# Kernel optimization log

Measured on AMD Instinct MI355X. Metric: run time of the kernel, lower is better.

The kernel has to match this reference:

```python
import jax, jax.numpy as jnp
import numpy as np

NEG_SLOPE = 0.2  # PyG GATv2Conv default

N_NODES = 10000
N_EDGES = 320000
DIM_IN = 128
DIM_H = 32
HEADS = 8
DIM_OUT = 32
HID = DIM_H * HEADS  # 256


def _gatv2(x, src, dst, Wl, Wr, att, bias, heads, ch, n):
    # x: [N, Fin]; src/dst: [E] (self-loops already included)
    xl = (x @ Wl).reshape(n, heads, ch)  # source-side transform
    xr = (x @ Wr).reshape(n, heads, ch)  # target-side transform
    e = jax.nn.leaky_relu(xl[src] + xr[dst], NEG_SLOPE)       # [E, H, C]
    score = jnp.einsum('ehc,hc->eh', e, att)                  # [E, H]
    m = jax.ops.segment_max(score, dst, num_segments=n)        # [N, H]
    ex = jnp.exp(score - m[dst])
    denom = jax.ops.segment_sum(ex, dst, num_segments=n)
    alpha = ex / (denom[dst] + 1e-16)                          # [E, H]
    out = jax.ops.segment_sum(alpha[:, :, None] * xl[src], dst, num_segments=n)
    return out.reshape(n, heads * ch) + bias


def setup_inputs() -> dict:
    key = jax.random.key(0)
    ks = jax.random.split(key, 16)
    x = jax.random.normal(ks[0], (N_NODES, DIM_IN), dtype=jnp.float32)
    edge_index = jax.random.randint(ks[1], (2, N_EDGES), 0, N_NODES, dtype=jnp.int64)

    def glorot(k, shape, fan_in):
        return jax.random.normal(k, shape, dtype=jnp.float32) * (1.0 / np.sqrt(fan_in))

    return {
        'x': x,
        'W1l': glorot(ks[2], (DIM_IN, HID), DIM_IN),
        'W1r': glorot(ks[3], (DIM_IN, HID), DIM_IN),
        'a1': glorot(ks[4], (HEADS, DIM_H), DIM_H),
        'b1': jnp.zeros((HID,), dtype=jnp.float32),
        'W2l': glorot(ks[5], (HID, HID), HID),
        'W2r': glorot(ks[6], (HID, HID), HID),
        'a2': glorot(ks[7], (HEADS, DIM_H), DIM_H),
        'b2': jnp.zeros((HID,), dtype=jnp.float32),
        'W3l': glorot(ks[8], (HID, DIM_OUT), HID),
        'W3r': glorot(ks[9], (HID, DIM_OUT), HID),
        'a3': glorot(ks[10], (1, DIM_OUT), DIM_OUT),
        'b3': jnp.zeros((DIM_OUT,), dtype=jnp.float32),
        'edge_index': edge_index,
    }


def reference(x, W1l, W1r, a1, b1, W2l, W2r, a2, b2, W3l, W3r, a3, b3, edge_index):
    n = x.shape[0]
    loops = jnp.arange(n, dtype=edge_index.dtype)
    src = jnp.concatenate([edge_index[0], loops])
    dst = jnp.concatenate([edge_index[1], loops])

    # eval mode: dropout(p=0.6) is identity
    h = _gatv2(x, src, dst, W1l, W1r, a1, b1, HEADS, DIM_H, n)
    h = jax.nn.relu(h)
    h_res = h
    h = _gatv2(h, src, dst, W2l, W2r, a2, b2, HEADS, DIM_H, n)
    h = h + h_res
    h = _gatv2(h, src, dst, W3l, W3r, a3, b3, 1, DIM_OUT, n)
    return h
```

## Files before the change

kernel.cpp:

```cpp
#include <hip/hip_runtime.h>

#define N_NODES 10000
#define N_EDGES 320000
#define E_TOT   (N_EDGES + N_NODES)
#define HID 256
#define NEG_SLOPE 0.2f
#define SLOTS 192

typedef __attribute__((ext_vector_type(8))) short short8;
typedef __attribute__((ext_vector_type(4))) float float4v;

__device__ int   g_cnt[N_NODES];
__device__ int   g_csr[(size_t)N_NODES * SLOTS];
__device__ __align__(16) float g_xl[(size_t)N_NODES * HID];
__device__ __align__(16) float g_xr[(size_t)N_NODES * HID];
__device__ __align__(16) float g_h1[(size_t)N_NODES * HID];
__device__ __align__(16) unsigned short g_xlb[(size_t)N_NODES * HID];
__device__ __align__(16) unsigned short g_abf[(size_t)N_NODES * 512];
__device__ __align__(16) unsigned short g_bp1a[16 * 8  * 64 * 8];
__device__ __align__(16) unsigned short g_bp2a[16 * 8  * 64 * 8];
__device__ __align__(16) unsigned short g_bp1b[16 * 16 * 64 * 8];
__device__ __align__(16) unsigned short g_bp2b[16 * 16 * 64 * 8];
__device__ __align__(16) unsigned short g_bp1c[2  * 16 * 64 * 8];
__device__ __align__(16) unsigned short g_bp2c[2  * 16 * 64 * 8];

#define LOG2E 1.44269504088896340736f

__device__ __forceinline__ unsigned short f2bf(float f) {
    unsigned int u = __float_as_uint(f);
    unsigned int r = (u + 0x7fffu + ((u >> 16) & 1u)) >> 16;
    return (unsigned short)r;
}
__device__ __forceinline__ float bf2f(unsigned short h) {
    return __uint_as_float(((unsigned int)h) << 16);
}
__device__ __forceinline__ unsigned int splitpack(float f) {
    unsigned short hi = f2bf(f);
    unsigned short lo = f2bf(f - bf2f(hi));
    return ((unsigned int)lo << 16) | hi;
}

__device__ __forceinline__ void packB(const float* __restrict__ B,
                                      unsigned short* __restrict__ Bp,
                                      int t, int nkc, int N) {
    int lane = t & 63;
    int kc   = (t >> 6) % nkc;
    int nt   = (t >> 6) / nkc;
    int n = nt * 16 + (lane & 15);
    int kbase = kc * 32 + (lane >> 4) * 8;
    #pragma unroll
    for (int j = 0; j < 8; ++j) {
        int kp = kbase + j;
        int k  = kp >> 1;
        float f = B[(size_t)k * N + n];
        unsigned short hi = f2bf(f);
        Bp[(size_t)t * 8 + j] = (kp & 1) ? f2bf(f - bf2f(hi)) : hi;
    }
}

__global__ __launch_bounds__(256) void k_prep(const float* __restrict__ W1l,
                                              const float* __restrict__ W1r,
                                              int* __restrict__ cnt) {
    const int S0 = 16 * 8 * 64;
    int t = blockIdx.x * blockDim.x + threadIdx.x;
    if (t < S0) {
        packB(W1l, g_bp1a, t, 8, 256);
        packB(W1r, g_bp2a, t, 8, 256);
    } else {
        int u = t - S0;
        if (u < N_NODES) cnt[u] = 0;
    }
}

#define FILL_BLOCKS  ((E_TOT + 255) / 256)
#define GEMM1_BLOCKS ((N_NODES + 31) / 32)
#define PACK2_BLOCKS ((16 * 16 * 64 + 2 * 16 * 64 + 255) / 256)
__global__ __launch_bounds__(256) void k_fill_gemm1(
    const int* __restrict__ ei,
    int* __restrict__ cnt, int* __restrict__ csr,
    const float4* __restrict__ A4,
    const short8* __restrict__ Bp1, const short8* __restrict__ Bp2,
    unsigned short* __restrict__ C1b,
    float* __restrict__ C2,
    const float* __restrict__ W2l, const float* __restrict__ W2r,
    const float* __restrict__ W3l, const float* __restrict__ W3r)
{
    if (blockIdx.x < FILL_BLOCKS) {
        int e = blockIdx.x * 256 + threadIdx.x;
        if (e < E_TOT) {
            int src, dst;
            if (e < N_EDGES) { src = ei[e]; dst = ei[N_EDGES + e]; }
            else             { src = dst = e - N_EDGES; }
            int pos = atomicAdd(&cnt[dst], 1);
            if (pos < SLOTS) csr[dst * SLOTS + pos] = src;
        }
        return;
    }
    if (blockIdx.x >= FILL_BLOCKS + GEMM1_BLOCKS) {
        const int S1 = 16 * 16 * 64;
        const int S2 = 2 * 16 * 64;
        int t = (blockIdx.x - FILL_BLOCKS - GEMM1_BLOCKS) * 256 + threadIdx.x;
        if (t < S1) {
            packB(W2l, g_bp1b, t, 16, 256);
            packB(W2r, g_bp2b, t, 16, 256);
        } else {
            int u = t - S1;
            if (u < S2) {
                packB(W3l, g_bp1c, u, 16, 32);
                packB(W3r, g_bp2c, u, 16, 32);
            }
        }
        return;
    }
    const int nkc = 8;
    int mt   = blockIdx.x - FILL_BLOCKS;
    int lane = threadIdx.x & 63;
    int wid  = threadIdx.x >> 6;
    int quad = lane >> 4;
    int col  = lane & 15;
    int r0 = mt * 32 + col;       if (r0 >= N_NODES) r0 = N_NODES - 1;
    int r1 = mt * 32 + 16 + col;  if (r1 >= N_NODES) r1 = N_NODES - 1;
    const float4* a0 = A4 + (size_t)r0 * 32 + quad;
    const float4* a1 = A4 + (size_t)r1 * 32 + quad;
    float4v acc[2][4][2];
    #pragma unroll
    for (int s = 0; s < 2; ++s)
        #pragma unroll
        for (int t = 0; t < 4; ++t) { acc[s][t][0] = (float4v)(0.f); acc[s][t][1] = (float4v)(0.f); }
    for (int kc = 0; kc < nkc; ++kc) {
        float4 v0 = a0[kc * 4];
        float4 v1 = a1[kc * 4];
        union { short8 s; unsigned int u[4]; } c0, c1;
        c0.u[0] = splitpack(v0.x); c0.u[1] = splitpack(v0.y);
        c0.u[2] = splitpack(v0.z); c0.u[3] = splitpack(v0.w);
        c1.u[0] = splitpack(v1.x); c1.u[1] = splitpack(v1.y);
        c1.u[2] = splitpack(v1.z); c1.u[3] = splitpack(v1.w);
        short8 A0 = c0.s, A1 = c1.s;
        #pragma unroll
        for (int t = 0; t < 4; ++t) {
            int nt = wid * 4 + t;
            size_t bi = ((size_t)(nt * nkc + kc)) * 64 + lane;
            short8 b1 = Bp1[bi];
            short8 b2 = Bp2[bi];
            acc[0][t][0] = __builtin_amdgcn_mfma_f32_16x16x32_bf16(A0, b1, acc[0][t][0], 0, 0, 0);
            acc[0][t][1] = __builtin_amdgcn_mfma_f32_16x16x32_bf16(A0, b2, acc[0][t][1], 0, 0, 0);
            acc[1][t][0] = __builtin_amdgcn_mfma_f32_16x16x32_bf16(A1, b1, acc[1][t][0], 0, 0, 0);
            acc[1][t][1] = __builtin_amdgcn_mfma_f32_16x16x32_bf16(A1, b2, acc[1][t][1], 0, 0, 0);
        }
    }
    #pragma unroll
    for (int s = 0; s < 2; ++s) {
        #pragma unroll
        for (int t = 0; t < 4; ++t) {
            int gc = (wid * 4 + t) * 16 + col;
            #pragma unroll
            for (int r = 0; r < 4; ++r) {
                int row = mt * 32 + s * 16 + quad * 4 + r;
                if (row < N_NODES) {
                    C1b[(size_t)row * 256 + gc] = f2bf(acc[s][t][0][r]);
                    C2[(size_t)row * 256 + gc]  = acc[s][t][1][r];
                }
            }
        }
    }
}

__global__ __launch_bounds__(256) void k_mgemm2(const short8* __restrict__ Af,
                                                const short8* __restrict__ Bp1,
                                                const short8* __restrict__ Bp2,
                                                unsigned short* __restrict__ C1b,
                                                float* __restrict__ C2,
                                                int Kp, int nkc) {
    int mt   = blockIdx.x;
    int lane = threadIdx.x & 63;
    int wid  = threadIdx.x >> 6;
    int quad = lane >> 4;
    int col  = lane & 15;
    int ks   = Kp >> 3;
    int r0 = mt * 32 + col;       if (r0 >= N_NODES) r0 = N_NODES - 1;
    int r1 = mt * 32 + 16 + col;  if (r1 >= N_NODES) r1 = N_NODES - 1;
    const short8* a0 = Af + (size_t)r0 * ks + quad;
    const short8* a1 = Af + (size_t)r1 * ks + quad;
    float4v acc[2][4][2];
    #pragma unroll
    for (int s = 0; s < 2; ++s)
        #pragma unroll
        for (int t = 0; t < 4; ++t) { acc[s][t][0] = (float4v)(0.f); acc[s][t][1] = (float4v)(0.f); }
    for (int kc = 0; kc < nkc; ++kc) {
        short8 A0 = a0[kc * 4];
        short8 A1 = a1[kc * 4];
        #pragma unroll
        for (int t = 0; t < 4; ++t) {
            int nt = wid * 4 + t;
            size_t bi = ((size_t)(nt * nkc + kc)) * 64 + lane;
            short8 b1 = Bp1[bi];
            short8 b2 = Bp2[bi];
            acc[0][t][0] = __builtin_amdgcn_mfma_f32_16x16x32_bf16(A0, b1, acc[0][t][0], 0, 0, 0);
            acc[0][t][1] = __builtin_amdgcn_mfma_f32_16x16x32_bf16(A0, b2, acc[0][t][1], 0, 0, 0);
            acc[1][t][0] = __builtin_amdgcn_mfma_f32_16x16x32_bf16(A1, b1, acc[1][t][0], 0, 0, 0);
            acc[1][t][1] = __builtin_amdgcn_mfma_f32_16x16x32_bf16(A1, b2, acc[1][t][1], 0, 0, 0);
        }
    }
    #pragma unroll
    for (int s = 0; s < 2; ++s) {
        #pragma unroll
        for (int t = 0; t < 4; ++t) {
            int gc = (wid * 4 + t) * 16 + col;
            #pragma unroll
            for (int r = 0; r < 4; ++r) {
                int row = mt * 32 + s * 16 + quad * 4 + r;
                if (row < N_NODES) {
                    C1b[(size_t)row * 256 + gc] = f2bf(acc[s][t][0][r]);
                    C2[(size_t)row * 256 + gc]  = acc[s][t][1][r];
                }
            }
        }
    }
}

__global__ __launch_bounds__(256) void k_mgemm32(const short8* __restrict__ Af,
                                                 const short8* __restrict__ Bp1,
                                                 const short8* __restrict__ Bp2,
                                                 float* __restrict__ C1,
                                                 float* __restrict__ C2) {
    int mt   = blockIdx.x;
    int lane = threadIdx.x & 63;
    int wid  = threadIdx.x >> 6;
    int quad = lane >> 4;
    int col  = lane & 15;
    int nt   = wid & 1;
    const short8* Bp = (wid < 2) ? Bp1 : Bp2;
    float* C = (wid < 2) ? C1 : C2;

    const short8* abase = Af + (size_t)(mt * 16 + col) * 64 + quad;
    float4v acc = (float4v)(0.f);
    #pragma unroll 4
    for (int kc = 0; kc < 16; ++kc) {
        short8 a = abase[kc * 4];
        short8 b = Bp[((size_t)(nt * 16 + kc)) * 64 + lane];
        acc = __builtin_amdgcn_mfma_f32_16x16x32_bf16(a, b, acc, 0, 0, 0);
    }
    #pragma unroll
    for (int r = 0; r < 4; ++r)
        C[(size_t)(mt * 16 + quad * 4 + r) * 32 + nt * 16 + col] = acc[r];
}

__global__ __launch_bounds__(256) void k_agg8(const unsigned short* __restrict__ xlb,
                                              const float4* __restrict__ xr4,
                                              const float4* __restrict__ att4,
                                              const float4* __restrict__ bias4,
                                              const int* __restrict__ cnt,
                                              const int* __restrict__ csr_src,
                                              const float4* __restrict__ res4,
                                              float4* __restrict__ out4,
                                              uint4* __restrict__ abf_out,
                                              int mode) {
    int node = blockIdx.x * 4 + (threadIdx.x >> 6);
    if (node >= N_NODES) return;
    int lane = threadIdx.x & 63;
    float4 xrv = xr4[(size_t)node * 64 + lane];
    float4 av  = att4[lane];
    av.x *= LOG2E; av.y *= LOG2E; av.z *= LOG2E; av.w *= LOG2E;
    int c = cnt[node]; if (c > SLOTS) c = SLOTS;
    int base0 = node * SLOTS;

    float s = 0.f;
    float4 acc = make_float4(0.f, 0.f, 0.f, 0.f);

    for (int base = 0; base < c; base += 64) {
        int li = base + lane;
        int idxv = csr_src[base0 + (li < c ? li : c - 1)];
        int m = c - base; if (m > 64) m = 64;
        for (int j0 = 0; j0 < m; j0 += 4) {
            int srcs[4];
            ushort4 uv[4];
            #pragma unroll
            for (int j = 0; j < 4; ++j)
                srcs[j] = __shfl(idxv, j0 + j);
            #pragma unroll
            for (int j = 0; j < 4; ++j)
                uv[j] = *(const ushort4*)(xlb + (size_t)srcs[j] * 256 + 4 * lane);
            #pragma unroll
            for (int j = 0; j < 4; ++j) {
                if (j0 + j < m) {
                    float4 xv;
                    xv.x = bf2f(uv[j].x); xv.y = bf2f(uv[j].y);
                    xv.z = bf2f(uv[j].z); xv.w = bf2f(uv[j].w);
                    float tx = xv.x + xrv.x, ty = xv.y + xrv.y;
                    float tz = xv.z + xrv.z, tw = xv.w + xrv.w;
                    float w = fmaxf(tx, NEG_SLOPE * tx) * av.x
                            + fmaxf(ty, NEG_SLOPE * ty) * av.y
                            + fmaxf(tz, NEG_SLOPE * tz) * av.z
                            + fmaxf(tw, NEG_SLOPE * tw) * av.w;
                    w += __shfl_xor(w, 1);
                    w += __shfl_xor(w, 2);
                    w += __shfl_xor(w, 4);
                    float p = exp2f(w);
                    s += p;
                    acc.x += p * xv.x;
                    acc.y += p * xv.y;
                    acc.z += p * xv.z;
                    acc.w += p * xv.w;
                }
            }
        }
    }

    float inv = 1.f / (s + 1e-16f);
    float4 bv = bias4[lane];
    float4 o;
    o.x = acc.x * inv + bv.x; o.y = acc.y * inv + bv.y;
    o.z = acc.z * inv + bv.z; o.w = acc.w * inv + bv.w;
    if (mode == 0) {
        o.x = fmaxf(o.x, 0.f); o.y = fmaxf(o.y, 0.f);
        o.z = fmaxf(o.z, 0.f); o.w = fmaxf(o.w, 0.f);
    } else {
        float4 r = res4[(size_t)node * 64 + lane];
        o.x += r.x; o.y += r.y; o.z += r.z; o.w += r.w;
    }
    if (out4) out4[(size_t)node * 64 + lane] = o;
    if (abf_out) {
        uint4 u;
        u.x = splitpack(o.x); u.y = splitpack(o.y);
        u.z = splitpack(o.z); u.w = splitpack(o.w);
        abf_out[(size_t)node * 64 + lane] = u;
    }
}

__global__ __launch_bounds__(256) void k_agg1(const float4* __restrict__ xl4,
                                              const float4* __restrict__ xr4,
                                              const float4* __restrict__ att4,
                                              const float4* __restrict__ bias4,
                                              const int* __restrict__ cnt,
                                              const int* __restrict__ csr_src,
                                              float4* __restrict__ out4) {
    int node = blockIdx.x * 4 + (threadIdx.x >> 6);
    if (node >= N_NODES) return;
    int lane = threadIdx.x & 63;
    int q = lane & 7;
    int grp = lane >> 3;
    float4 xrv = xr4[(size_t)node * 8 + q];
    float4 av  = att4[q];
    av.x *= LOG2E; av.y *= LOG2E; av.z *= LOG2E; av.w *= LOG2E;
    int c = cnt[node]; if (c > SLOTS) c = SLOTS;
    int start = node * SLOTS, end = start + c;
    float s = 0.f;
    float4 acc = make_float4(0.f, 0.f, 0.f, 0.f);
    for (int i = start + grp; i < end; i += 8) {
        int src = csr_src[i];
        float4 xv = xl4[(size_t)src * 8 + q];
        float tx = xv.x + xrv.x, ty = xv.y + xrv.y;
        float tz = xv.z + xrv.z, tw = xv.w + xrv.w;
        float w = fmaxf(tx, NEG_SLOPE * tx) * av.x
                + fmaxf(ty, NEG_SLOPE * ty) * av.y
                + fmaxf(tz, NEG_SLOPE * tz) * av.z
                + fmaxf(tw, NEG_SLOPE * tw) * av.w;
        w += __shfl_xor(w, 1);
        w += __shfl_xor(w, 2);
        w += __shfl_xor(w, 4);
        float p = exp2f(w);
        s += p;
        acc.x += p * xv.x;
        acc.y += p * xv.y;
        acc.z += p * xv.z;
        acc.w += p * xv.w;
    }
    #pragma unroll
    for (int off = 8; off < 64; off <<= 1) {
        s     += __shfl_xor(s, off);
        acc.x += __shfl_xor(acc.x, off);
        acc.y += __shfl_xor(acc.y, off);
        acc.z += __shfl_xor(acc.z, off);
        acc.w += __shfl_xor(acc.w, off);
    }
    if (grp == 0) {
        float inv = 1.f / (s + 1e-16f);
        float4 bv = bias4[q];
        float4 o;
        o.x = acc.x * inv + bv.x; o.y = acc.y * inv + bv.y;
        o.z = acc.z * inv + bv.z; o.w = acc.w * inv + bv.w;
        out4[(size_t)node * 8 + q] = o;
    }
}


extern "C" void kernel_launch(void* const* d_in, const int* in_sizes, int n_in,
                              void* d_out, int out_size, void* d_ws, size_t ws_size,
                              hipStream_t stream) {
    const float* x   = (const float*)d_in[0];
    const float* W1l = (const float*)d_in[1];
    const float* W1r = (const float*)d_in[2];
    const float* a1  = (const float*)d_in[3];
    const float* b1  = (const float*)d_in[4];
    const float* W2l = (const float*)d_in[5];
    const float* W2r = (const float*)d_in[6];
    const float* a2  = (const float*)d_in[7];
    const float* b2  = (const float*)d_in[8];
    const float* W3l = (const float*)d_in[9];
    const float* W3r = (const float*)d_in[10];
    const float* a3  = (const float*)d_in[11];
    const float* b3  = (const float*)d_in[12];
    const int*   ei  = (const int*)d_in[13];
    float* out = (float*)d_out;

    int *cnt, *csr;
    float *xl, *xr, *h1;
    unsigned short *xlb, *abf, *bp1a, *bp2a, *bp1b, *bp2b, *bp1c, *bp2c;
    hipGetSymbolAddress((void**)&cnt,    HIP_SYMBOL(g_cnt));
    hipGetSymbolAddress((void**)&csr,    HIP_SYMBOL(g_csr));
    hipGetSymbolAddress((void**)&xl,     HIP_SYMBOL(g_xl));
    hipGetSymbolAddress((void**)&xr,     HIP_SYMBOL(g_xr));
    hipGetSymbolAddress((void**)&h1,     HIP_SYMBOL(g_h1));
    hipGetSymbolAddress((void**)&xlb,    HIP_SYMBOL(g_xlb));
    hipGetSymbolAddress((void**)&abf,    HIP_SYMBOL(g_abf));
    hipGetSymbolAddress((void**)&bp1a,   HIP_SYMBOL(g_bp1a));
    hipGetSymbolAddress((void**)&bp2a,   HIP_SYMBOL(g_bp2a));
    hipGetSymbolAddress((void**)&bp1b,   HIP_SYMBOL(g_bp1b));
    hipGetSymbolAddress((void**)&bp2b,   HIP_SYMBOL(g_bp2b));
    hipGetSymbolAddress((void**)&bp1c,   HIP_SYMBOL(g_bp1c));
    hipGetSymbolAddress((void**)&bp2c,   HIP_SYMBOL(g_bp2c));

    k_prep<<<(16 * 8 * 64 + N_NODES + 255) / 256, 256, 0, stream>>>(W1l, W1r, cnt);

    k_fill_gemm1<<<FILL_BLOCKS + GEMM1_BLOCKS + PACK2_BLOCKS, 256, 0, stream>>>(
        ei, cnt, csr, (const float4*)x,
        (const short8*)bp1a, (const short8*)bp2a, xlb, xr,
        W2l, W2r, W3l, W3r);

    k_agg8<<<(N_NODES + 3) / 4, 256, 0, stream>>>(xlb, (const float4*)xr,
                                        (const float4*)a1, (const float4*)b1,
                                        cnt, csr, nullptr, (float4*)h1,
                                        (uint4*)abf, 0);

    k_mgemm2<<<(N_NODES + 31) / 32, 256, 0, stream>>>((const short8*)abf,
                                                      (const short8*)bp1b, (const short8*)bp2b,
                                                      xlb, xr, 512, 16);

    k_agg8<<<(N_NODES + 3) / 4, 256, 0, stream>>>(xlb, (const float4*)xr,
                                        (const float4*)a2, (const float4*)b2,
                                        cnt, csr, (const float4*)h1, nullptr,
                                        (uint4*)abf, 1);

    k_mgemm32<<<N_NODES / 16, 256, 0, stream>>>((const short8*)abf,
                                                (const short8*)bp1c, (const short8*)bp2c,
                                                xl, xr);

    k_agg1<<<(N_NODES + 3) / 4, 256, 0, stream>>>((const float4*)xl, (const float4*)xr,
                                                  (const float4*)a3, (const float4*)b3,
                                                  cnt, csr, (float4*)out);
}
```

Measured before the change: 227.1 us.

## Fuse GAT aggregation with following layer GEMM via shared-memory tile

```diff
diff --git a/kernel.cpp b/kernel.cpp
--- a/kernel.cpp
+++ b/kernel.cpp
@@ -16,7 +16,7 @@
 __device__ __align__(16) float g_xr[(size_t)N_NODES * HID];
 __device__ __align__(16) float g_h1[(size_t)N_NODES * HID];
 __device__ __align__(16) unsigned short g_xlb[(size_t)N_NODES * HID];
-__device__ __align__(16) unsigned short g_abf[(size_t)N_NODES * 512];
+__device__ __align__(16) unsigned short g_xlb2[(size_t)N_NODES * HID];
 __device__ __align__(16) unsigned short g_bp1a[16 * 8  * 64 * 8];
 __device__ __align__(16) unsigned short g_bp2a[16 * 8  * 64 * 8];
 __device__ __align__(16) unsigned short g_bp1b[16 * 16 * 64 * 8];
@@ -165,165 +165,151 @@
     }
 }
 
-__global__ __launch_bounds__(256) void k_mgemm2(const short8* __restrict__ Af,
-                                                const short8* __restrict__ Bp1,
-                                                const short8* __restrict__ Bp2,
+__global__ __launch_bounds__(512) void k_aggemm(const unsigned short* __restrict__ xlb,
+                                                const float4* __restrict__ xr4,
+                                                const float4* __restrict__ att4,
+                                                const float4* __restrict__ bias4,
+                                                const int* __restrict__ cnt,
+                                                const int* __restrict__ csr_src,
+                                                const float4* __restrict__ res4,
+                                                float4* __restrict__ h1out,
+                                                const short8* __restrict__ BpA,
+                                                const short8* __restrict__ BpB,
                                                 unsigned short* __restrict__ C1b,
                                                 float* __restrict__ C2,
-                                                int Kp, int nkc) {
-    int mt   = blockIdx.x;
+                                                float* __restrict__ C1f,
+                                                int mode) {
+    __shared__ uint4 sp[16][64];
     int lane = threadIdx.x & 63;
     int wid  = threadIdx.x >> 6;
     int quad = lane >> 4;
     int col  = lane & 15;
-    int ks   = Kp >> 3;
-    int r0 = mt * 32 + col;       if (r0 >= N_NODES) r0 = N_NODES - 1;
-    int r1 = mt * 32 + 16 + col;  if (r1 >= N_NODES) r1 = N_NODES - 1;
-    const short8* a0 = Af + (size_t)r0 * ks + quad;
-    const short8* a1 = Af + (size_t)r1 * ks + quad;
-    float4v acc[2][4][2];
-    #pragma unroll
-    for (int s = 0; s < 2; ++s)
-        #pragma unroll
-        for (int t = 0; t < 4; ++t) { acc[s][t][0] = (float4v)(0.f); acc[s][t][1] = (float4v)(0.f); }
-    for (int kc = 0; kc < nkc; ++kc) {
-        short8 A0 = a0[kc * 4];
-        short8 A1 = a1[kc * 4];
-        #pragma unroll
-        for (int t = 0; t < 4; ++t) {
-            int nt = wid * 4 + t;
-            size_t bi = ((size_t)(nt * nkc + kc)) * 64 + lane;
-            short8 b1 = Bp1[bi];
-            short8 b2 = Bp2[bi];
-            acc[0][t][0] = __builtin_amdgcn_mfma_f32_16x16x32_bf16(A0, b1, acc[0][t][0], 0, 0, 0);
-            acc[0][t][1] = __builtin_amdgcn_mfma_f32_16x16x32_bf16(A0, b2, acc[0][t][1], 0, 0, 0);
-            acc[1][t][0] = __builtin_amdgcn_mfma_f32_16x16x32_bf16(A1, b1, acc[1][t][0], 0, 0, 0);
-            acc[1][t][1] = __builtin_amdgcn_mfma_f32_16x16x32_bf16(A1, b2, acc[1][t][1], 0, 0, 0);
-        }
-    }
-    #pragma unroll
-    for (int s = 0; s < 2; ++s) {
-        #pragma unroll
-        for (int t = 0; t < 4; ++t) {
-            int gc = (wid * 4 + t) * 16 + col;
-            #pragma unroll
-            for (int r = 0; r < 4; ++r) {
-                int row = mt * 32 + s * 16 + quad * 4 + r;
-                if (row < N_NODES) {
-                    C1b[(size_t)row * 256 + gc] = f2bf(acc[s][t][0][r]);
-                    C2[(size_t)row * 256 + gc]  = acc[s][t][1][r];
+
+    float4 av = att4[lane];
+    av.x *= LOG2E; av.y *= LOG2E; av.z *= LOG2E; av.w *= LOG2E;
+    float4 bv = bias4[lane];
+
+    for (int nn = 0; nn < 2; ++nn) {
+        int row  = wid * 2 + nn;
+        int node = blockIdx.x * 16 + row;
+        float4 xrv = xr4[(size_t)node * 64 + lane];
+        int c = cnt[node]; if (c > SLOTS) c = SLOTS;
+        int base0 = node * SLOTS;
+
+        float s = 0.f;
+        float4 acc = make_float4(0.f, 0.f, 0.f, 0.f);
+
+        for (int base = 0; base < c; base += 64) {
+            int li = base + lane;
+            int idxv = csr_src[base0 + (li < c ? li : c - 1)];
+            int m = c - base; if (m > 64) m = 64;
+            for (int j0 = 0; j0 < m; j0 += 4) {
+                int srcs[4];
+                ushort4 uv[4];
+                #pragma unroll
+                for (int j = 0; j < 4; ++j)
+                    srcs[j] = __shfl(idxv, j0 + j);
+                #pragma unroll
+                for (int j = 0; j < 4; ++j)
+                    uv[j] = *(const ushort4*)(xlb + (size_t)srcs[j] * 256 + 4 * lane);
+                #pragma unroll
+                for (int j = 0; j < 4; ++j) {
+                    if (j0 + j < m) {
+                        float4 xv;
+                        xv.x = bf2f(uv[j].x); xv.y = bf2f(uv[j].y);
+                        xv.z = bf2f(uv[j].z); xv.w = bf2f(uv[j].w);
+                        float tx = xv.x + xrv.x, ty = xv.y + xrv.y;
+                        float tz = xv.z + xrv.z, tw = xv.w + xrv.w;
+                        float w = fmaxf(tx, NEG_SLOPE * tx) * av.x
+                                + fmaxf(ty, NEG_SLOPE * ty) * av.y
+                                + fmaxf(tz, NEG_SLOPE * tz) * av.z
+                                + fmaxf(tw, NEG_SLOPE * tw) * av.w;
+                        w += __shfl_xor(w, 1);
+                        w += __shfl_xor(w, 2);
+                        w += __shfl_xor(w, 4);
+                        float p = exp2f(w);
+                        s += p;
+                        acc.x += p * xv.x;
+                        acc.y += p * xv.y;
+                        acc.z += p * xv.z;
+                        acc.w += p * xv.w;
+                    }
                 }
             }
         }
-    }
-}
-
-__global__ __launch_bounds__(256) void k_mgemm32(const short8* __restrict__ Af,
-                                                 const short8* __restrict__ Bp1,
-                                                 const short8* __restrict__ Bp2,
-                                                 float* __restrict__ C1,
-                                                 float* __restrict__ C2) {
-    int mt   = blockIdx.x;
-    int lane = threadIdx.x & 63;
-    int wid  = threadIdx.x >> 6;
-    int quad = lane >> 4;
-    int col  = lane & 15;
-    int nt   = wid & 1;
-    const short8* Bp = (wid < 2) ? Bp1 : Bp2;
-    float* C = (wid < 2) ? C1 : C2;
-
-    const short8* abase = Af + (size_t)(mt * 16 + col) * 64 + quad;
-    float4v acc = (float4v)(0.f);
-    #pragma unroll 4
-    for (int kc = 0; kc < 16; ++kc) {
-        short8 a = abase[kc * 4];
-        short8 b = Bp[((size_t)(nt * 16 + kc)) * 64 + lane];
-        acc = __builtin_amdgcn_mfma_f32_16x16x32_bf16(a, b, acc, 0, 0, 0);
-    }
-    #pragma unroll
-    for (int r = 0; r < 4; ++r)
-        C[(size_t)(mt * 16 + quad * 4 + r) * 32 + nt * 16 + col] = acc[r];
-}
-
-__global__ __launch_bounds__(256) void k_agg8(const unsigned short* __restrict__ xlb,
-                                              const float4* __restrict__ xr4,
-                                              const float4* __restrict__ att4,
-                                              const float4* __restrict__ bias4,
-                                              const int* __restrict__ cnt,
-                                              const int* __restrict__ csr_src,
-                                              const float4* __restrict__ res4,
-                                              float4* __restrict__ out4,
-                                              uint4* __restrict__ abf_out,
-                                              int mode) {
-    int node = blockIdx.x * 4 + (threadIdx.x >> 6);
-    if (node >= N_NODES) return;
-    int lane = threadIdx.x & 63;
-    float4 xrv = xr4[(size_t)node * 64 + lane];
-    float4 av  = att4[lane];
-    av.x *= LOG2E; av.y *= LOG2E; av.z *= LOG2E; av.w *= LOG2E;
-    int c = cnt[node]; if (c > SLOTS) c = SLOTS;
-    int base0 = node * SLOTS;
-
-    float s = 0.f;
-    float4 acc = make_float4(0.f, 0.f, 0.f, 0.f);
-
-    for (int base = 0; base < c; base += 64) {
-        int li = base + lane;
-        int idxv = csr_src[base0 + (li < c ? li : c - 1)];
-        int m = c - base; if (m > 64) m = 64;
-        for (int j0 = 0; j0 < m; j0 += 4) {
-            int srcs[4];
-            ushort4 uv[4];
-            #pragma unroll
-            for (int j = 0; j < 4; ++j)
-                srcs[j] = __shfl(idxv, j0 + j);
-            #pragma unroll
-            for (int j = 0; j < 4; ++j)
-                uv[j] = *(const ushort4*)(xlb + (size_t)srcs[j] * 256 + 4 * lane);
-            #pragma unroll
-            for (int j = 0; j < 4; ++j) {
-                if (j0 + j < m) {
-                    float4 xv;
-                    xv.x = bf2f(uv[j].x); xv.y = bf2f(uv[j].y);
-                    xv.z = bf2f(uv[j].z); xv.w = bf2f(uv[j].w);
-                    float tx = xv.x + xrv.x, ty = xv.y + xrv.y;
-                    float tz = xv.z + xrv.z, tw = xv.w + xrv.w;
-                    float w = fmaxf(tx, NEG_SLOPE * tx) * av.x
-                            + fmaxf(ty, NEG_SLOPE * ty) * av.y
-                            + fmaxf(tz, NEG_SLOPE * tz) * av.z
-                            + fmaxf(tw, NEG_SLOPE * tw) * av.w;
-                    w += __shfl_xor(w, 1);
-                    w += __shfl_xor(w, 2);
-                    w += __shfl_xor(w, 4);
-                    float p = exp2f(w);
-                    s += p;
-                    acc.x += p * xv.x;
-                    acc.y += p * xv.y;
-                    acc.z += p * xv.z;
-                    acc.w += p * xv.w;
-                }
-            }
-        }
-    }
-
-    float inv = 1.f / (s + 1e-16f);
-    float4 bv = bias4[lane];
-    float4 o;
-    o.x = acc.x * inv + bv.x; o.y = acc.y * inv + bv.y;
-    o.z = acc.z * inv + bv.z; o.w = acc.w * inv + bv.w;
-    if (mode == 0) {
-        o.x = fmaxf(o.x, 0.f); o.y = fmaxf(o.y, 0.f);
-        o.z = fmaxf(o.z, 0.f); o.w = fmaxf(o.w, 0.f);
-    } else {
-        float4 r = res4[(size_t)node * 64 + lane];
-        o.x += r.x; o.y += r.y; o.z += r.z; o.w += r.w;
-    }
-    if (out4) out4[(size_t)node * 64 + lane] = o;
-    if (abf_out) {
+
+        float inv = 1.f / (s + 1e-16f);
+        float4 o;
+        o.x = acc.x * inv + bv.x; o.y = acc.y * inv + bv.y;
+        o.z = acc.z * inv + bv.z; o.w = acc.w * inv + bv.w;
+        if (mode == 0) {
+            o.x = fmaxf(o.x, 0.f); o.y = fmaxf(o.y, 0.f);
+            o.z = fmaxf(o.z, 0.f); o.w = fmaxf(o.w, 0.f);
+            h1out[(size_t)node * 64 + lane] = o;
+        } else {
+            float4 r = res4[(size_t)node * 64 + lane];
+            o.x += r.x; o.y += r.y; o.z += r.z; o.w += r.w;
+        }
         uint4 u;
         u.x = splitpack(o.x); u.y = splitpack(o.y);
         u.z = splitpack(o.z); u.w = splitpack(o.w);
-        abf_out[(size_t)node * 64 + lane] = u;
+        sp[row][lane ^ (row & 7)] = u;
+    }
+    __syncthreads();
+
+    int arow = lane & 15;
+    if (mode == 0) {
+        const short8* Bsel[4];
+        int ntv[4];
+        #pragma unroll
+        for (int t = 0; t < 4; ++t) {
+            int tile = wid * 4 + t;
+            Bsel[t] = (tile < 16) ? BpA : BpB;
+            ntv[t] = tile & 15;
+        }
+        float4v acc[4];
+        #pragma unroll
+        for (int t = 0; t < 4; ++t) acc[t] = (float4v)(0.f);
+        for (int kc = 0; kc < 16; ++kc) {
+            union { uint4 q; short8 s; } a;
+            a.q = sp[arow][(kc * 4 + quad) ^ (arow & 7)];
+            #pragma unroll
+            for (int t = 0; t < 4; ++t) {
+                short8 b = Bsel[t][((size_t)(ntv[t] * 16 + kc)) * 64 + lane];
+                acc[t] = __builtin_amdgcn_mfma_f32_16x16x32_bf16(a.s, b, acc[t], 0, 0, 0);
+            }
+        }
+        #pragma unroll
+        for (int t = 0; t < 4; ++t) {
+            int tile = wid * 4 + t;
+            int gc = ntv[t] * 16 + col;
+            #pragma unroll
+            for (int r = 0; r < 4; ++r) {
+                int node = blockIdx.x * 16 + quad * 4 + r;
+                if (tile < 16) C1b[(size_t)node * 256 + gc] = f2bf(acc[t][r]);
+                else           C2[(size_t)node * 256 + gc]  = acc[t][r];
+            }
+        }
+    } else {
+        if (wid < 4) {
+            int mat = wid >> 1;
+            int nt  = wid & 1;
+            const short8* Bp = mat ? BpB : BpA;
+            float4v acc = (float4v)(0.f);
+            for (int kc = 0; kc < 16; ++kc) {
+                union { uint4 q; short8 s; } a;
+                a.q = sp[arow][(kc * 4 + quad) ^ (arow & 7)];
+                short8 b = Bp[((size_t)(nt * 16 + kc)) * 64 + lane];
+                acc = __builtin_amdgcn_mfma_f32_16x16x32_bf16(a.s, b, acc, 0, 0, 0);
+            }
+            float* C = mat ? C2 : C1f;
+            int gc = nt * 16 + col;
+            #pragma unroll
+            for (int r = 0; r < 4; ++r) {
+                int node = blockIdx.x * 16 + quad * 4 + r;
+                C[(size_t)node * 32 + gc] = acc[r];
+            }
+        }
     }
 }
 
@@ -405,14 +391,14 @@
 
     int *cnt, *csr;
     float *xl, *xr, *h1;
-    unsigned short *xlb, *abf, *bp1a, *bp2a, *bp1b, *bp2b, *bp1c, *bp2c;
+    unsigned short *xlb, *xlb2, *bp1a, *bp2a, *bp1b, *bp2b, *bp1c, *bp2c;
     hipGetSymbolAddress((void**)&cnt,    HIP_SYMBOL(g_cnt));
     hipGetSymbolAddress((void**)&csr,    HIP_SYMBOL(g_csr));
     hipGetSymbolAddress((void**)&xl,     HIP_SYMBOL(g_xl));
     hipGetSymbolAddress((void**)&xr,     HIP_SYMBOL(g_xr));
     hipGetSymbolAddress((void**)&h1,     HIP_SYMBOL(g_h1));
     hipGetSymbolAddress((void**)&xlb,    HIP_SYMBOL(g_xlb));
-    hipGetSymbolAddress((void**)&abf,    HIP_SYMBOL(g_abf));
+    hipGetSymbolAddress((void**)&xlb2,   HIP_SYMBOL(g_xlb2));
     hipGetSymbolAddress((void**)&bp1a,   HIP_SYMBOL(g_bp1a));
     hipGetSymbolAddress((void**)&bp2a,   HIP_SYMBOL(g_bp2a));
     hipGetSymbolAddress((void**)&bp1b,   HIP_SYMBOL(g_bp1b));
@@ -420,6 +406,9 @@
     hipGetSymbolAddress((void**)&bp1c,   HIP_SYMBOL(g_bp1c));
     hipGetSymbolAddress((void**)&bp2c,   HIP_SYMBOL(g_bp2c));
 
+    float* xl3 = xr;
+    float* xr3 = xr + (size_t)N_NODES * 32;
+
     k_prep<<<(16 * 8 * 64 + N_NODES + 255) / 256, 256, 0, stream>>>(W1l, W1r, cnt);
 
     k_fill_gemm1<<<FILL_BLOCKS + GEMM1_BLOCKS + PACK2_BLOCKS, 256, 0, stream>>>(
@@ -427,25 +416,19 @@
         (const short8*)bp1a, (const short8*)bp2a, xlb, xr,
         W2l, W2r, W3l, W3r);
 
-    k_agg8<<<(N_NODES + 3) / 4, 256, 0, stream>>>(xlb, (const float4*)xr,
-                                        (const float4*)a1, (const float4*)b1,
-                                        cnt, csr, nullptr, (float4*)h1,
-                                        (uint4*)abf, 0);
-
-    k_mgemm2<<<(N_NODES + 31) / 32, 256, 0, stream>>>((const short8*)abf,
-                                                      (const short8*)bp1b, (const short8*)bp2b,
-                                                      xlb, xr, 512, 16);
-
-    k_agg8<<<(N_NODES + 3) / 4, 256, 0, stream>>>(xlb, (const float4*)xr,
-                                        (const float4*)a2, (const float4*)b2,
-                                        cnt, csr, (const float4*)h1, nullptr,
-                                        (uint4*)abf, 1);
-
-    k_mgemm32<<<N_NODES / 16, 256, 0, stream>>>((const short8*)abf,
-                                                (const short8*)bp1c, (const short8*)bp2c,
-                                                xl, xr);
-
-    k_agg1<<<(N_NODES + 3) / 4, 256, 0, stream>>>((const float4*)xl, (const float4*)xr,
+    k_aggemm<<<N_NODES / 16, 512, 0, stream>>>(
+        xlb, (const float4*)xr, (const float4*)a1, (const float4*)b1,
+        cnt, csr, nullptr, (float4*)h1,
+        (const short8*)bp1b, (const short8*)bp2b,
+        xlb2, xl, nullptr, 0);
+
+    k_aggemm<<<N_NODES / 16, 512, 0, stream>>>(
+        xlb2, (const float4*)xl, (const float4*)a2, (const float4*)b2,
+        cnt, csr, (const float4*)h1, nullptr,
+        (const short8*)bp1c, (const short8*)bp2c,
+        nullptr, xr3, xl3, 1);
+
+    k_agg1<<<(N_NODES + 3) / 4, 256, 0, stream>>>((const float4*)xl3, (const float4*)xr3,
                                                   (const float4*)a3, (const float4*)b3,
                                                   cnt, csr, (float4*)out);
 }
```

New measurement: 250.2 us. 1.1x slower.
